# Optimization experiments

Measured on AMD Instinct MI355X. Metric: run time of the kernel, lower is better.

## Reference

```python
import jax, jax.numpy as jnp
import numpy as np

B = 512          # batch of graphs
N_LOCAL = 33     # local nodes per graph
NPG = 34         # nodes per graph (1 global + 33 local)
C = 768          # feat_dims[-1] (global feature channels)
FEAT = 1152      # concat_dim = sum(feat_dims) = 384 + 768
GPD = 2048       # global_proj_dim
HID = 1024       # hidden_dim_proj
H = 8            # num_heads
AD = 64          # att_dim
LLM = 4096       # llama_dim
DEG = 8          # average degree of random graph
E_PER = NPG * DEG
NT = B * NPG     # total nodes


def setup_inputs() -> dict:
    key = jax.random.key(0)
    ks = jax.random.split(key, 16)
    sc = 0.02
    local_features = jax.random.normal(ks[0], (B, 1, N_LOCAL, FEAT), jnp.float32)
    global_features = jax.random.normal(ks[1], (B, C, 8, 8, 4), jnp.float32)
    # random batched graph: edges stay within each graph, offset by 34*b
    src = jax.random.randint(ks[2], (B, E_PER), 0, NPG)
    dst = jax.random.randint(ks[3], (B, E_PER), 0, NPG)
    off = (jnp.arange(B, dtype=jnp.int32) * NPG)[:, None]
    edge_index = jnp.stack([(src + off).reshape(-1), (dst + off).reshape(-1)]).astype(jnp.int32)
    return {
        "local_features": local_features,
        "global_features": global_features,
        "edge_index": edge_index,
        "W1g": jax.random.normal(ks[4], (32 * C, GPD), jnp.float32) * sc,
        "b1g": jnp.zeros((GPD,), jnp.float32),
        "W2g": jax.random.normal(ks[5], (GPD, FEAT), jnp.float32) * sc,
        "b2g": jnp.zeros((FEAT,), jnp.float32),
        "Wp": jax.random.normal(ks[6], (FEAT, HID), jnp.float32) * sc,
        "bp": jnp.zeros((HID,), jnp.float32),
        "Wg": jax.random.normal(ks[7], (HID, H * AD), jnp.float32) * sc,
        "a_src": jax.random.normal(ks[8], (H, AD), jnp.float32) * sc,
        "a_dst": jax.random.normal(ks[9], (H, AD), jnp.float32) * sc,
        "Wllm": jax.random.normal(ks[10], (H * AD, LLM), jnp.float32) * sc,
        "bllm": jnp.zeros((LLM,), jnp.float32),
    }


def reference(local_features, global_features, edge_index,
              W1g, b1g, W2g, b2g, Wp, bp, Wg, a_src, a_dst, Wllm, bllm):
    # AdaptiveAvgPool3d((4,4,2)) on (8,8,4): exact 2x2x2 mean pooling
    x = global_features.reshape(B, C, 4, 2, 4, 2, 2, 2).mean(axis=(3, 5, 7))
    x = x.reshape(B, -1)                                   # [B, 32*C]
    out_global = jax.nn.relu(x @ W1g + b1g) @ W2g + b2g    # [B, FEAT]
    # concat global node with local nodes -> [B, 34, FEAT] -> flatten batched graph
    nodes = jnp.concatenate([out_global[:, None, :], local_features[:, 0]], axis=1)
    nodes = nodes.reshape(NT, FEAT)

    # GAT layer: hidden projection, per-head features, edge attention
    h = jax.nn.relu(nodes @ Wp + bp)                       # [NT, HID]
    z = (h @ Wg).reshape(NT, H, AD)                        # [NT, H, AD]
    s, d = edge_index[0], edge_index[1]
    e = jax.nn.leaky_relu(
        jnp.einsum('ehd,hd->eh', z[s], a_src) + jnp.einsum('ehd,hd->eh', z[d], a_dst),
        negative_slope=0.2)                                # [E, H]
    m = jax.ops.segment_max(e, d, num_segments=NT)
    m = jnp.where(jnp.isfinite(m), m, 0.0)                 # guard isolated nodes
    ex = jnp.exp(e - m[d])
    den = jax.ops.segment_sum(ex, d, num_segments=NT)
    alpha = ex / (den[d] + 1e-9)                           # neighbor softmax per dst
    agg = jax.ops.segment_sum(alpha[:, :, None] * z[s], d, num_segments=NT)  # [NT, H, AD]
    gnn_feats = agg.reshape(NT, H * AD)

    out = gnn_feats.reshape(B, NPG, H * AD) @ Wllm + bllm  # [B, 34, LLM]
    return out
```

## Files before the change

### kernel.cpp

```cpp
#include <hip/hip_runtime.h>
#include <hip/hip_bf16.h>
#include <math.h>

#define BB    512
#define NPG   34
#define NT    17408
#define FEAT  1152
#define GPD   2048
#define HID   1024
#define NH    8
#define AD    64
#define HA    512
#define LLM   4096
#define EPG   272
#define NE    139264
#define C32   24576
#define CC    768

#define AS3 __attribute__((address_space(3)))
#define AS1 __attribute__((address_space(1)))

typedef __attribute__((ext_vector_type(8))) short short8v;
typedef __attribute__((ext_vector_type(4))) float f32x4;

__device__ __forceinline__ ushort f2bf(float f) {
    __hip_bfloat16 h = __float2bfloat16(f);
    return __builtin_bit_cast(ushort, h);
}

__device__ __forceinline__ void d_transpose(const float* __restrict__ W, ushort* __restrict__ WT,
                                            int R, int Cn, int bx, int by,
                                            float (*tile)[33], int tid) {
    int c0 = bx * 32, r0 = by * 32;
    int tc = tid & 31, tr = tid >> 5;
#pragma unroll
    for (int i = 0; i < 4; i++)
        tile[tr + i * 8][tc] = W[(size_t)(r0 + tr + i * 8) * Cn + c0 + tc];
    __syncthreads();
#pragma unroll
    for (int it = 0; it < 2; it++) {
        int p = tid + it * 256;
        int c = p >> 4, pr = (p & 15) << 1;
        ushort2 v;
        v.x = f2bf(tile[pr][c]);
        v.y = f2bf(tile[pr + 1][c]);
        *(ushort2*)&WT[(size_t)(c0 + c) * R + r0 + pr] = v;
    }
}

__device__ __forceinline__ void d_pool(const float* __restrict__ gf, ushort* __restrict__ outB,
                                       int blk, int tid) {
    int t = blk * 256 + tid;
    int q = t & 15; int bc = t >> 4;
    int dO = q >> 2, hO = q & 3;
    const float* p = gf + (size_t)bc * 256 + dO * 64 + hO * 8;
    float4 r00 = *(const float4*)(p);
    float4 r01 = *(const float4*)(p + 4);
    float4 r10 = *(const float4*)(p + 32);
    float4 r11 = *(const float4*)(p + 36);
    float o0 = (r00.x + r00.y + r01.x + r01.y + r10.x + r10.y + r11.x + r11.y) * 0.125f;
    float o1 = (r00.z + r00.w + r01.z + r01.w + r10.z + r10.w + r11.z + r11.w) * 0.125f;
    int b = bc / CC, c = bc % CC;
    ushort2 v; v.x = f2bf(o0); v.y = f2bf(o1);
    *(ushort2*)(outB + (size_t)b * C32 + c * 32 + dO * 8 + hO * 2) = v;
}

__global__ __launch_bounds__(256) void k_prep(
    const float* __restrict__ W1g, ushort* __restrict__ W1gT,
    const float* __restrict__ W2g, ushort* __restrict__ W2gT,
    const float* __restrict__ Wp,  ushort* __restrict__ WpT,
    const float* __restrict__ Wg,  ushort* __restrict__ WgT,
    const float* __restrict__ Wllm, ushort* __restrict__ WllmT,
    const float* __restrict__ gf,  ushort* __restrict__ poolB) {
    __shared__ float tile[32][33];
    int blk = blockIdx.x, tid = threadIdx.x;
    if (blk < 49152) {
        d_transpose(W1g, W1gT, C32, GPD, blk & 63, blk >> 6, tile, tid);
    } else if (blk < 51456) {
        int l = blk - 49152; d_transpose(W2g, W2gT, GPD, FEAT, l % 36, l / 36, tile, tid);
    } else if (blk < 52608) {
        int l = blk - 51456; d_transpose(Wp, WpT, FEAT, HID, l & 31, l >> 5, tile, tid);
    } else if (blk < 53120) {
        int l = blk - 52608; d_transpose(Wg, WgT, HID, HA, l & 15, l >> 4, tile, tid);
    } else if (blk < 55168) {
        int l = blk - 53120; d_transpose(Wllm, WllmT, HA, LLM, l & 127, l >> 7, tile, tid);
    } else {
        d_pool(gf, poolB, blk - 55168, tid);
    }
}

#define GLDS(gp, lp) __builtin_amdgcn_global_load_lds((const AS1 void*)(gp), (AS3 void*)(lp), 16, 0, 0)
#define STAGE_A(buf, h, tt) { \
    const ushort* s_ = gAs + (size_t)(tt) * 64 + (size_t)(2 * (h)) * rK; \
    ushort* d_ = lds + (buf) * 32768 + (2 * (h)) * 4096 + (w << 9); \
    GLDS(s_, d_); GLDS(s_ + rK, d_ + 4096); }
#define STAGE_B(buf, h, tt) { \
    const ushort* s_ = gBs + (size_t)(tt) * 64 + (size_t)(2 * (h)) * rK; \
    ushort* d_ = lds + (buf) * 32768 + 16384 + (2 * (h)) * 4096 + (w << 9); \
    GLDS(s_, d_); GLDS(s_ + rK, d_ + 4096); }
#define DSRA(BO, mh) { _Pragma("unroll") for (int mf = 0; mf < 4; mf++) { \
    const ushort* p_ = lds + (BO) + aBase + ((mh) * 64 + mf * 16) * 64; \
    aF[mf][0] = *(const short8v*)(p_ + k0s); \
    aF[mf][1] = *(const short8v*)(p_ + k1s); } }
#define DSRB(BO, nh, BF) { _Pragma("unroll") for (int nf = 0; nf < 2; nf++) { \
    const ushort* p_ = lds + (BO) + bBase + ((nh) * 32 + nf * 16) * 64; \
    BF[nf][0] = *(const short8v*)(p_ + k0s); \
    BF[nf][1] = *(const short8v*)(p_ + k1s); } }
#define MM(mh, nh, BF) { \
    asm volatile("s_waitcnt lgkmcnt(0)" ::: "memory"); \
    __builtin_amdgcn_sched_barrier(0); \
    __builtin_amdgcn_s_setprio(1); \
    _Pragma("unroll") for (int mf = 0; mf < 4; mf++) \
    _Pragma("unroll") for (int nf = 0; nf < 2; nf++) { \
        acc[(mh)*4+mf][(nh)*2+nf] = __builtin_amdgcn_mfma_f32_16x16x32_bf16(aF[mf][0], BF[nf][0], acc[(mh)*4+mf][(nh)*2+nf], 0, 0, 0); \
        acc[(mh)*4+mf][(nh)*2+nf] = __builtin_amdgcn_mfma_f32_16x16x32_bf16(aF[mf][1], BF[nf][1], acc[(mh)*4+mf][(nh)*2+nf], 0, 0, 0); } \
    __builtin_amdgcn_s_setprio(0); }
#define BAR __builtin_amdgcn_s_barrier()
#define VMW4 { asm volatile("s_waitcnt vmcnt(4)" ::: "memory"); __builtin_amdgcn_sched_barrier(0); }

template<bool SPLITK, bool BIAS, bool RELU, bool OUTBF>
__global__ __launch_bounds__(512, 2) void k_gemm256(
    const ushort* __restrict__ A, const ushort* __restrict__ BT,
    const float* __restrict__ bias, void* __restrict__ Cout,
    int M, int N, int K, int kChunk) {
    __shared__ ushort lds[65536];
    const int t = threadIdx.x;
    const int w = t >> 6, l = t & 63;
    const int wm = w >> 2, wn = w & 3;
    const int gx = gridDim.x;
    const int nwg = gx * gridDim.y;
    const int id = blockIdx.y * gx + blockIdx.x;
    const int qx = nwg >> 3, rx = nwg & 7;
    const int xcd = id & 7, pos = id >> 3;
    const int nid = (xcd < rx ? xcd * (qx + 1) : rx * (qx + 1) + (xcd - rx) * qx) + pos;
    const int m0 = (nid / gx) * 256, n0 = (nid % gx) * 256;
    const int kBase = SPLITK ? blockIdx.z * kChunk : 0;
    const int NTt = (SPLITK ? kChunk : K) / 64;

    const int rowLo = t >> 3;
    const int keSrc = ((t & 7) << 3) ^ (((rowLo >> 2) & 1) << 5) ^ (((rowLo >> 3) & 1) << 4);
    const ushort* gAs = A + (size_t)(m0 + rowLo) * K + kBase + keSrc;
    const ushort* gBs = BT + (size_t)(n0 + rowLo) * K + kBase + keSrc;
    const size_t rK = (size_t)64 * K;

    const int fcol = l & 15, fk = (l >> 4) << 3;
    const int flipR = (((l >> 2) & 1) << 5) | (((l >> 3) & 1) << 4);
    const int k0s = fk ^ flipR;
    const int k1s = fk ^ 32 ^ flipR;
    const int aBase = (wm * 128 + fcol) * 64;
    const int bBase = 16384 + (wn * 64 + fcol) * 64;

    short8v aF[4][2], bF0[2][2], bF1[2][2];
    f32x4 acc[8][4] = {};

    STAGE_B(0, 0, 0); STAGE_B(0, 1, 0); STAGE_A(0, 0, 0); STAGE_A(0, 1, 0);
    STAGE_B(1, 0, 1); STAGE_B(1, 1, 1);
    VMW4;
    BAR;

    const int NITER = NTt >> 1;
    for (int it = 0; it < NITER; ++it) {
        const int t1 = 2 * it + 1;
        const int t2r = 2 * it + 2, t3r = 2 * it + 3;
        const int t2 = t2r < NTt ? t2r : 0;
        const int t3 = t3r < NTt ? t3r : 0;
        DSRA(0, 0); DSRB(0, 0, bF0); STAGE_A(1, 0, t1);
        BAR; MM(0, 0, bF0); BAR;
        DSRB(0, 1, bF1); STAGE_A(1, 1, t1);
        BAR; MM(0, 1, bF1); BAR;
        DSRA(0, 1); STAGE_B(0, 0, t2);
        BAR; MM(1, 1, bF1); BAR;
        STAGE_B(0, 1, t2); VMW4;
        BAR; MM(1, 0, bF0); BAR;
        DSRA(32768, 0); DSRB(32768, 0, bF0); STAGE_A(0, 0, t2);
        BAR; MM(0, 0, bF0); BAR;
        DSRB(32768, 1, bF1); STAGE_A(0, 1, t2);
        BAR; MM(0, 1, bF1); BAR;
        DSRA(32768, 1); STAGE_B(1, 0, t3);
        BAR; MM(1, 1, bF1); BAR;
        STAGE_B(1, 1, t3); VMW4;
        BAR; MM(1, 0, bF0); BAR;
    }
    asm volatile("s_waitcnt vmcnt(0)" ::: "memory");
    BAR;

    const int orow = (l >> 4) << 2;
    float* eph = ((float*)lds) + w * 2176;
    const int ecol = (l & 15) << 2;
    const int erow4 = l >> 4;
#pragma unroll
    for (int pass = 0; pass < 4; pass++) {
#pragma unroll
        for (int mi = 0; mi < 2; mi++) {
            int mf = pass * 2 + mi;
#pragma unroll
            for (int nf = 0; nf < 4; nf++)
#pragma unroll
                for (int r = 0; r < 4; r++)
                    eph[(mi * 16 + orow + r) * 68 + nf * 16 + fcol] = acc[mf][nf][r];
        }
#pragma unroll
        for (int g = 0; g < 8; g++) {
            int lrow = g * 4 + erow4;
            f32x4 v = *(f32x4*)&eph[lrow * 68 + ecol];
            int row = m0 + wm * 128 + pass * 32 + lrow;
            int col = n0 + wn * 64 + ecol;
            if (BIAS) {
                float4 bb = *(const float4*)(bias + col);
                v[0] += bb.x; v[1] += bb.y; v[2] += bb.z; v[3] += bb.w;
            }
            if (RELU) {
#pragma unroll
                for (int q = 0; q < 4; q++) v[q] = v[q] > 0.f ? v[q] : 0.f;
            }
            if (OUTBF) {
                ushort4 u;
                u.x = f2bf(v[0]); u.y = f2bf(v[1]); u.z = f2bf(v[2]); u.w = f2bf(v[3]);
                *(ushort4*)&((ushort*)Cout)[(size_t)row * N + col] = u;
            } else {
                size_t off = (size_t)row * N + col;
                if (SPLITK) off += (size_t)blockIdx.z * (size_t)M * N;
                float4 fv = {v[0], v[1], v[2], v[3]};
                *(float4*)&((float*)Cout)[off] = fv;
            }
        }
    }
}

template<bool SPLITK, bool BIAS, bool RELU, bool OUTBF>
__global__ __launch_bounds__(256) void k_gemm_bf(
    const ushort* __restrict__ A, const ushort* __restrict__ BT,
    const float* __restrict__ bias, void* __restrict__ Cout,
    int M, int N, int K, int kChunk) {
    __shared__ ushort lA[128 * 32];
    __shared__ ushort lB[128 * 32];
    const int t = threadIdx.x;
    const int w = t >> 6, l = t & 63;
    const int m0 = blockIdx.y * 128, n0 = blockIdx.x * 128;
    const int kLen = SPLITK ? kChunk : K;
    const int k0 = SPLITK ? blockIdx.z * kChunk : 0;
    const int srow = w * 16 + (l >> 2);
    const int skq = (l & 3) << 3;
    const ushort* gA = A + (size_t)(m0 + srow) * K + k0 + skq;
    const ushort* gB = BT + (size_t)(n0 + srow) * K + k0 + skq;
    ushort* lA0 = lA + w * 512;
    ushort* lB0 = lB + w * 512;
    const size_t str64 = (size_t)64 * K;
    const int wr = (w >> 1) << 6, wc = (w & 1) << 6;
    const int fcol = l & 15, fk = (l >> 4) << 3;

    f32x4 acc[4][4] = {};
    for (int kk = 0; kk < kLen; kk += 32) {
        __syncthreads();
        GLDS(gA + kk,         lA0);
        GLDS(gA + kk + str64, lA0 + 2048);
        GLDS(gB + kk,         lB0);
        GLDS(gB + kk + str64, lB0 + 2048);
        __syncthreads();
        short8v a[4], b[4];
#pragma unroll
        for (int f = 0; f < 4; f++) {
            a[f] = *(const short8v*)(lA + (wr + f * 16 + fcol) * 32 + fk);
            b[f] = *(const short8v*)(lB + (wc + f * 16 + fcol) * 32 + fk);
        }
#pragma unroll
        for (int i = 0; i < 4; i++)
#pragma unroll
            for (int j = 0; j < 4; j++)
                acc[i][j] = __builtin_amdgcn_mfma_f32_16x16x32_bf16(a[i], b[j], acc[i][j], 0, 0, 0);
    }
    const int orow = (l >> 4) << 2;
#pragma unroll
    for (int i = 0; i < 4; i++) {
#pragma unroll
        for (int j = 0; j < 4; j++) {
            int col = n0 + wc + j * 16 + fcol;
            float bv = BIAS ? bias[col] : 0.f;
#pragma unroll
            for (int r = 0; r < 4; r++) {
                int row = m0 + wr + i * 16 + orow + r;
                float v = acc[i][j][r] + bv;
                if (RELU) v = v > 0.f ? v : 0.f;
                if (OUTBF) {
                    ((ushort*)Cout)[(size_t)row * N + col] = f2bf(v);
                } else {
                    size_t off = (size_t)row * N + col;
                    if (SPLITK) off += (size_t)blockIdx.z * (size_t)M * N;
                    ((float*)Cout)[off] = v;
                }
            }
        }
    }
}

template<int NP, bool RELU>
__global__ __launch_bounds__(256) void k_red(const float* __restrict__ part,
                                             const float* __restrict__ bias,
                                             ushort* __restrict__ outB,
                                             int N, int stride) {
    int i = blockIdx.x * 256 + threadIdx.x;
    float s = bias[i % N];
#pragma unroll
    for (int q = 0; q < NP; q++) s += part[i + (size_t)q * stride];
    if (RELU) s = s > 0.f ? s : 0.f;
    outB[i] = f2bf(s);
}

__global__ __launch_bounds__(256) void k_nodes(const ushort* __restrict__ outgB,
                                               const float* __restrict__ locf,
                                               ushort* __restrict__ nodesB) {
    int idx = blockIdx.x * 256 + threadIdx.x;
    int node = idx / 144, cc = idx - node * 144;
    int b = node / NPG, j = node - b * NPG;
    int c = cc * 8;
    ushort* dst = nodesB + (size_t)node * FEAT + c;
    if (j == 0) {
        *(uint4*)dst = *(const uint4*)(outgB + (size_t)b * FEAT + c);
    } else {
        const float* s = locf + ((size_t)b * 33 + (j - 1)) * FEAT + c;
        float4 v0 = *(const float4*)s, v1 = *(const float4*)(s + 4);
        ushort u[8] = {f2bf(v0.x), f2bf(v0.y), f2bf(v0.z), f2bf(v0.w),
                       f2bf(v1.x), f2bf(v1.y), f2bf(v1.z), f2bf(v1.w)};
        *(uint4*)dst = *(uint4*)u;
    }
}

__global__ __launch_bounds__(256) void k_gat(const int* __restrict__ es, const int* __restrict__ ed,
                                             const float* __restrict__ z,
                                             const float* __restrict__ a_src,
                                             const float* __restrict__ a_dst,
                                             ushort* __restrict__ gnnB) {
    __shared__ float zt[NPG][520];
    __shared__ float sps[NPG][NH], spd[NPG][NH], sm[NPG][NH], sden[NPG][NH];
    __shared__ float esc[EPG][NH];
    __shared__ int srcl[EPG], dll[EPG], order[EPG], cnt[NPG], bstart[NPG + 1];
    int b = blockIdx.x, t = threadIdx.x;
    for (int i = t; i < NPG * 128; i += 256) {
        int n = i >> 7, c4 = (i & 127) << 2;
        *(float4*)&zt[n][c4] = *(const float4*)&z[((size_t)b * NPG + n) * HA + c4];
    }
    for (int e = t; e < EPG; e += 256) {
        srcl[e] = es[b * EPG + e] - b * NPG;
        dll[e]  = ed[b * EPG + e] - b * NPG;
    }
    if (t < NPG) cnt[t] = 0;
    __syncthreads();
    {
        int wv = t >> 6, l = t & 63;
        for (int n = wv; n < NPG; n += 4) {
            float s[NH], d[NH];
#pragma unroll
            for (int i = 0; i < NH; i++) {
                float zv = zt[n][i * 64 + l];
                s[i] = zv * a_src[i * 64 + l];
                d[i] = zv * a_dst[i * 64 + l];
            }
#pragma unroll
            for (int i = 0; i < NH; i++) {
#pragma unroll
                for (int off = 32; off > 0; off >>= 1) {
                    s[i] += __shfl_xor(s[i], off);
                    d[i] += __shfl_xor(d[i], off);
                }
            }
            if (l == 0) {
#pragma unroll
                for (int i = 0; i < NH; i++) { sps[n][i] = s[i]; spd[n][i] = d[i]; }
            }
        }
    }
    for (int e = t; e < EPG; e += 256) atomicAdd(&cnt[dll[e]], 1);
    __syncthreads();
    if (t == 0) {
        int s = 0;
        for (int n = 0; n < NPG; n++) { bstart[n] = s; s += cnt[n]; cnt[n] = bstart[n]; }
        bstart[NPG] = s;
        for (int e = 0; e < EPG; e++) order[cnt[dll[e]]++] = e;
    }
    __syncthreads();
    for (int i = t; i < EPG * NH; i += 256) {
        int e = i >> 3, h = i & 7;
        float sc = sps[srcl[e]][h] + spd[dll[e]][h];
        esc[e][h] = sc > 0.f ? sc : 0.2f * sc;
    }
    __syncthreads();
    for (int i = t; i < NPG * NH; i += 256) {
        int n = i >> 3, h = i & 7;
        float m = -INFINITY;
        for (int j = bstart[n]; j < bstart[n + 1]; j++) m = fmaxf(m, esc[order[j]][h]);
        if (m == -INFINITY) m = 0.f;
        float den = 0.f;
        for (int j = bstart[n]; j < bstart[n + 1]; j++) den += expf(esc[order[j]][h] - m);
        sm[n][h] = m; sden[n][h] = den;
    }
    __syncthreads();
    for (int i = t; i < EPG * NH; i += 256) {
        int e = i >> 3, h = i & 7;
        esc[e][h] = expf(esc[e][h] - sm[dll[e]][h]) / (sden[dll[e]][h] + 1e-9f);
    }
    __syncthreads();
    for (int c = t; c < NPG * 64; c += 256) {
        int n = c >> 6, rem = c & 63, h = rem >> 3, d0 = (rem & 7) << 3;
        float acc[8] = {};
        for (int j = bstart[n]; j < bstart[n + 1]; j++) {
            int e = order[j];
            float a = esc[e][h];
            const float* zp = &zt[srcl[e]][h * 64 + d0];
#pragma unroll
            for (int q = 0; q < 8; q++) acc[q] = fmaf(a, zp[q], acc[q]);
        }
        ushort u[8];
#pragma unroll
        for (int q = 0; q < 8; q++) u[q] = f2bf(acc[q]);
        *(uint4*)&gnnB[((size_t)b * NPG + n) * HA + h * 64 + d0] = *(uint4*)u;
    }
}

extern "C" void kernel_launch(void* const* d_in, const int* in_sizes, int n_in,
                              void* d_out, int out_size, void* d_ws, size_t ws_size,
                              hipStream_t stream) {
    const float* locf  = (const float*)d_in[0];
    const float* gf    = (const float*)d_in[1];
    const int*   ei    = (const int*)d_in[2];
    const float* W1g   = (const float*)d_in[3];
    const float* b1g   = (const float*)d_in[4];
    const float* W2g   = (const float*)d_in[5];
    const float* b2g   = (const float*)d_in[6];
    const float* Wp    = (const float*)d_in[7];
    const float* bp    = (const float*)d_in[8];
    const float* Wg    = (const float*)d_in[9];
    const float* a_src = (const float*)d_in[10];
    const float* a_dst = (const float*)d_in[11];
    const float* Wllm  = (const float*)d_in[12];
    const float* bllm  = (const float*)d_in[13];
    float* out = (float*)d_out;
    float* ws  = (float*)d_ws;
    const int* es = ei;
    const int* ed = ei + NE;

    float*  z      = out;
    ushort* W1gT   = (ushort*)(out + 8912896);
    ushort* hB     = (ushort*)(out + 8912896);
    ushort* poolB  = (ushort*)(out + 34078720);
    float*  part1  = out + 40370176;
    ushort* nodesB = (ushort*)(out + 40370176);
    ushort* g1B    = (ushort*)(out + 57147392);
    ushort* W2gT   = (ushort*)(out + 57671680);
    ushort* WpT    = (ushort*)(out + 58851328);
    ushort* WgT    = (ushort*)(out + 59441152);
    ushort* outgB  = (ushort*)(out + 59703296);
    float*  part2  = out + 59998208;
    ushort* WllmT = (ushort*)ws;
    ushort* gnnB  = (ushort*)(ws + 1048576);

    k_prep<<<79744, 256, 0, stream>>>(W1g, W1gT, W2g, W2gT, Wp, WpT, Wg, WgT,
                                      Wllm, WllmT, gf, poolB);
    k_gemm256<true, false, false, false><<<dim3(8, 2, 16), 512, 0, stream>>>(
        poolB, W1gT, nullptr, part1, 512, GPD, C32, 1536);
    k_red<16, true><<<4096, 256, 0, stream>>>(part1, b1g, g1B, GPD, 1048576);
    k_gemm_bf<true, false, false, false><<<dim3(9, 4, 4), 256, 0, stream>>>(
        g1B, W2gT, nullptr, part2, 512, FEAT, GPD, 512);
    k_red<4, false><<<2304, 256, 0, stream>>>(part2, b2g, outgB, FEAT, 589824);
    k_nodes<<<9792, 256, 0, stream>>>(outgB, locf, nodesB);
    k_gemm256<false, true, true, true><<<dim3(4, 68), 512, 0, stream>>>(
        nodesB, WpT, bp, hB, NT, HID, FEAT, 0);
    k_gemm256<false, false, false, false><<<dim3(2, 68), 512, 0, stream>>>(
        hB, WgT, nullptr, z, NT, HA, HID, 0);
    k_gat<<<BB, 256, 0, stream>>>(es, ed, z, a_src, a_dst, gnnB);
    k_gemm256<false, true, false, false><<<dim3(16, 68), 512, 0, stream>>>(
        gnnB, WllmT, bllm, out, NT, LLM, HA, 0);
}
```

Measured before the change: 595.2 us.

## Fuse z projection GEMM into GAT kernel and remap split-K block order

Replaces the separate h@Wg GEMM and the fp32 z round trip through global memory with an in-block MFMA projection. Each graph's 34 rows are multiplied by WgT directly into LDS inside a new 512-thread GAT kernel. The split-K GEMM also gets a z-major XCD-aware block remapping so that K-chunk blocks sharing output tiles are grouped. The fused projection pads 34 rows to 48 and streams WgT from global per block without LDS staging, so it wastes some MFMA work and re-reads WgT 512 times.

```diff
diff --git a/kernel.cpp b/kernel.cpp
--- a/kernel.cpp
+++ b/kernel.cpp
@@ -118,7 +118,7 @@
 #define BAR __builtin_amdgcn_s_barrier()
 #define VMW4 { asm volatile("s_waitcnt vmcnt(4)" ::: "memory"); __builtin_amdgcn_sched_barrier(0); }
 
-template<bool SPLITK, bool BIAS, bool RELU, bool OUTBF>
+template<bool SPLITK, bool ZMAJ, bool BIAS, bool RELU, bool OUTBF>
 __global__ __launch_bounds__(512, 2) void k_gemm256(
     const ushort* __restrict__ A, const ushort* __restrict__ BT,
     const float* __restrict__ bias, void* __restrict__ Cout,
@@ -127,14 +127,29 @@
     const int t = threadIdx.x;
     const int w = t >> 6, l = t & 63;
     const int wm = w >> 2, wn = w & 3;
-    const int gx = gridDim.x;
-    const int nwg = gx * gridDim.y;
-    const int id = blockIdx.y * gx + blockIdx.x;
-    const int qx = nwg >> 3, rx = nwg & 7;
-    const int xcd = id & 7, pos = id >> 3;
-    const int nid = (xcd < rx ? xcd * (qx + 1) : rx * (qx + 1) + (xcd - rx) * qx) + pos;
-    const int m0 = (nid / gx) * 256, n0 = (nid % gx) * 256;
-    const int kBase = SPLITK ? blockIdx.z * kChunk : 0;
+    int m0, n0, kz = 0;
+    {
+        const int gx = gridDim.x, gy = gridDim.y;
+        if (ZMAJ) {
+            const int nwg = gx * gy * gridDim.z;
+            const int id = (blockIdx.z * gx + blockIdx.x) * gy + blockIdx.y;
+            const int qc = nwg >> 3, rc = nwg & 7;
+            const int xcd = id & 7, pos = id >> 3;
+            const int nid = (xcd < rc ? xcd * (qc + 1) : rc * (qc + 1) + (xcd - rc) * qc) + pos;
+            const int y = nid % gy; const int r2 = nid / gy;
+            const int x = r2 % gx; kz = r2 / gx;
+            m0 = y * 256; n0 = x * 256;
+        } else {
+            const int nwg = gx * gy;
+            const int id = blockIdx.y * gx + blockIdx.x;
+            const int qc = nwg >> 3, rc = nwg & 7;
+            const int xcd = id & 7, pos = id >> 3;
+            const int nid = (xcd < rc ? xcd * (qc + 1) : rc * (qc + 1) + (xcd - rc) * qc) + pos;
+            m0 = (nid / gx) * 256; n0 = (nid % gx) * 256;
+            kz = blockIdx.z;
+        }
+    }
+    const int kBase = SPLITK ? kz * kChunk : 0;
     const int NTt = (SPLITK ? kChunk : K) / 64;
 
     const int rowLo = t >> 3;
@@ -219,7 +234,7 @@
                 *(ushort4*)&((ushort*)Cout)[(size_t)row * N + col] = u;
             } else {
                 size_t off = (size_t)row * N + col;
-                if (SPLITK) off += (size_t)blockIdx.z * (size_t)M * N;
+                if (SPLITK) off += (size_t)kz * (size_t)M * N;
                 float4 fv = {v[0], v[1], v[2], v[3]};
                 *(float4*)&((float*)Cout)[off] = fv;
             }
@@ -325,51 +340,89 @@
     }
 }
 
-__global__ __launch_bounds__(256) void k_gat(const int* __restrict__ es, const int* __restrict__ ed,
-                                             const float* __restrict__ z,
-                                             const float* __restrict__ a_src,
-                                             const float* __restrict__ a_dst,
-                                             ushort* __restrict__ gnnB) {
-    __shared__ float zt[NPG][520];
-    __shared__ float sps[NPG][NH], spd[NPG][NH], sm[NPG][NH], sden[NPG][NH];
+__global__ __launch_bounds__(512) void k_zgat(const int* __restrict__ es, const int* __restrict__ ed,
+                                              const ushort* __restrict__ hB,
+                                              const ushort* __restrict__ WgT,
+                                              const float* __restrict__ a_src,
+                                              const float* __restrict__ a_dst,
+                                              ushort* __restrict__ gnnB) {
+    __shared__ float zt[NPG][521];
+    __shared__ float sps[NPG][NH], spd[NPG][NH], smx[NPG][NH], sden[NPG][NH];
     __shared__ float esc[EPG][NH];
     __shared__ int srcl[EPG], dll[EPG], order[EPG], cnt[NPG], bstart[NPG + 1];
-    int b = blockIdx.x, t = threadIdx.x;
-    for (int i = t; i < NPG * 128; i += 256) {
-        int n = i >> 7, c4 = (i & 127) << 2;
-        *(float4*)&zt[n][c4] = *(const float4*)&z[((size_t)b * NPG + n) * HA + c4];
-    }
-    for (int e = t; e < EPG; e += 256) {
+    const int b = blockIdx.x, t = threadIdx.x;
+    const int w = t >> 6, l = t & 63;
+    const int lm = l & 15, lh = l >> 4;
+
+    f32x4 acc[3][4] = {};
+    const ushort* hrow[3];
+    bool hval[3];
+#pragma unroll
+    for (int mi = 0; mi < 3; mi++) {
+        int row = mi * 16 + lm;
+        hval[mi] = row < NPG;
+        hrow[mi] = hB + ((size_t)b * NPG + (hval[mi] ? row : 0)) * HID + lh * 8;
+    }
+    const ushort* brow[4];
+#pragma unroll
+    for (int q = 0; q < 4; q++)
+        brow[q] = WgT + (size_t)((w * 4 + q) * 16 + lm) * HID + lh * 8;
+    const short8v zerov = {};
+#pragma unroll 2
+    for (int ks = 0; ks < 32; ks++) {
+        const int kb = ks * 32;
+        short8v af[3], bf[4];
+#pragma unroll
+        for (int mi = 0; mi < 3; mi++) {
+            short8v v = *(const short8v*)(hrow[mi] + kb);
+            af[mi] = hval[mi] ? v : zerov;
+        }
+#pragma unroll
+        for (int q = 0; q < 4; q++) bf[q] = *(const short8v*)(brow[q] + kb);
+#pragma unroll
+        for (int mi = 0; mi < 3; mi++)
+#pragma unroll
+            for (int q = 0; q < 4; q++)
+                acc[mi][q] = __builtin_amdgcn_mfma_f32_16x16x32_bf16(af[mi], bf[q], acc[mi][q], 0, 0, 0);
+    }
+#pragma unroll
+    for (int mi = 0; mi < 3; mi++)
+#pragma unroll
+        for (int q = 0; q < 4; q++)
+#pragma unroll
+            for (int r = 0; r < 4; r++) {
+                int m = mi * 16 + lh * 4 + r;
+                if (m < NPG) zt[m][(w * 4 + q) * 16 + lm] = acc[mi][q][r];
+            }
+    for (int e = t; e < EPG; e += 512) {
         srcl[e] = es[b * EPG + e] - b * NPG;
         dll[e]  = ed[b * EPG + e] - b * NPG;
     }
     if (t < NPG) cnt[t] = 0;
     __syncthreads();
-    {
-        int wv = t >> 6, l = t & 63;
-        for (int n = wv; n < NPG; n += 4) {
-            float s[NH], d[NH];
-#pragma unroll
-            for (int i = 0; i < NH; i++) {
-                float zv = zt[n][i * 64 + l];
-                s[i] = zv * a_src[i * 64 + l];
-                d[i] = zv * a_dst[i * 64 + l];
+
+    for (int n = w; n < NPG; n += 8) {
+        float s[NH], d[NH];
+#pragma unroll
+        for (int i = 0; i < NH; i++) {
+            float zv = zt[n][i * 64 + l];
+            s[i] = zv * a_src[i * 64 + l];
+            d[i] = zv * a_dst[i * 64 + l];
+        }
+#pragma unroll
+        for (int i = 0; i < NH; i++) {
+#pragma unroll
+            for (int off = 32; off > 0; off >>= 1) {
+                s[i] += __shfl_xor(s[i], off);
+                d[i] += __shfl_xor(d[i], off);
             }
-#pragma unroll
-            for (int i = 0; i < NH; i++) {
-#pragma unroll
-                for (int off = 32; off > 0; off >>= 1) {
-                    s[i] += __shfl_xor(s[i], off);
-                    d[i] += __shfl_xor(d[i], off);
-                }
-            }
-            if (l == 0) {
-#pragma unroll
-                for (int i = 0; i < NH; i++) { sps[n][i] = s[i]; spd[n][i] = d[i]; }
-            }
-        }
-    }
-    for (int e = t; e < EPG; e += 256) atomicAdd(&cnt[dll[e]], 1);
+        }
+        if (l == 0) {
+#pragma unroll
+            for (int i = 0; i < NH; i++) { sps[n][i] = s[i]; spd[n][i] = d[i]; }
+        }
+    }
+    for (int e = t; e < EPG; e += 512) atomicAdd(&cnt[dll[e]], 1);
     __syncthreads();
     if (t == 0) {
         int s = 0;
@@ -378,40 +431,40 @@
         for (int e = 0; e < EPG; e++) order[cnt[dll[e]]++] = e;
     }
     __syncthreads();
-    for (int i = t; i < EPG * NH; i += 256) {
+    for (int i = t; i < EPG * NH; i += 512) {
         int e = i >> 3, h = i & 7;
         float sc = sps[srcl[e]][h] + spd[dll[e]][h];
         esc[e][h] = sc > 0.f ? sc : 0.2f * sc;
     }
     __syncthreads();
-    for (int i = t; i < NPG * NH; i += 256) {
+    for (int i = t; i < NPG * NH; i += 512) {
         int n = i >> 3, h = i & 7;
         float m = -INFINITY;
         for (int j = bstart[n]; j < bstart[n + 1]; j++) m = fmaxf(m, esc[order[j]][h]);
         if (m == -INFINITY) m = 0.f;
         float den = 0.f;
         for (int j = bstart[n]; j < bstart[n + 1]; j++) den += expf(esc[order[j]][h] - m);
-        sm[n][h] = m; sden[n][h] = den;
-    }
-    __syncthreads();
-    for (int i = t; i < EPG * NH; i += 256) {
+        smx[n][h] = m; sden[n][h] = den;
+    }
+    __syncthreads();
+    for (int i = t; i < EPG * NH; i += 512) {
         int e = i >> 3, h = i & 7;
-        esc[e][h] = expf(esc[e][h] - sm[dll[e]][h]) / (sden[dll[e]][h] + 1e-9f);
-    }
-    __syncthreads();
-    for (int c = t; c < NPG * 64; c += 256) {
+        esc[e][h] = expf(esc[e][h] - smx[dll[e]][h]) / (sden[dll[e]][h] + 1e-9f);
+    }
+    __syncthreads();
+    for (int c = t; c < NPG * 64; c += 512) {
         int n = c >> 6, rem = c & 63, h = rem >> 3, d0 = (rem & 7) << 3;
-        float acc[8] = {};
+        float a8[8] = {};
         for (int j = bstart[n]; j < bstart[n + 1]; j++) {
             int e = order[j];
             float a = esc[e][h];
             const float* zp = &zt[srcl[e]][h * 64 + d0];
 #pragma unroll
-            for (int q = 0; q < 8; q++) acc[q] = fmaf(a, zp[q], acc[q]);
+            for (int q = 0; q < 8; q++) a8[q] = fmaf(a, zp[q], a8[q]);
         }
         ushort u[8];
 #pragma unroll
-        for (int q = 0; q < 8; q++) u[q] = f2bf(acc[q]);
+        for (int q = 0; q < 8; q++) u[q] = f2bf(a8[q]);
         *(uint4*)&gnnB[((size_t)b * NPG + n) * HA + h * 64 + d0] = *(uint4*)u;
     }
 }
@@ -438,7 +491,6 @@
     const int* es = ei;
     const int* ed = ei + NE;
 
-    float*  z      = out;
     ushort* W1gT   = (ushort*)(out + 8912896);
     ushort* hB     = (ushort*)(out + 8912896);
     ushort* poolB  = (ushort*)(out + 34078720);
@@ -455,18 +507,16 @@
 
     k_prep<<<79744, 256, 0, stream>>>(W1g, W1gT, W2g, W2gT, Wp, WpT, Wg, WgT,
                                       Wllm, WllmT, gf, poolB);
-    k_gemm256<true, false, false, false><<<dim3(8, 2, 16), 512, 0, stream>>>(
+    k_gemm256<true, true, false, false, false><<<dim3(8, 2, 16), 512, 0, stream>>>(
         poolB, W1gT, nullptr, part1, 512, GPD, C32, 1536);
     k_red<16, true><<<4096, 256, 0, stream>>>(part1, b1g, g1B, GPD, 1048576);
     k_gemm_bf<true, false, false, false><<<dim3(9, 4, 4), 256, 0, stream>>>(
         g1B, W2gT, nullptr, part2, 512, FEAT, GPD, 512);
     k_red<4, false><<<2304, 256, 0, stream>>>(part2, b2g, outgB, FEAT, 589824);
     k_nodes<<<9792, 256, 0, stream>>>(outgB, locf, nodesB);
-    k_gemm256<false, true, true, true><<<dim3(4, 68), 512, 0, stream>>>(
+    k_gemm256<false, false, true, true, true><<<dim3(4, 68), 512, 0, stream>>>(
         nodesB, WpT, bp, hB, NT, HID, FEAT, 0);
-    k_gemm256<false, false, false, false><<<dim3(2, 68), 512, 0, stream>>>(
-        hB, WgT, nullptr, z, NT, HA, HID, 0);
-    k_gat<<<BB, 256, 0, stream>>>(es, ed, z, a_src, a_dst, gnnB);
-    k_gemm256<false, true, false, false><<<dim3(16, 68), 512, 0, stream>>>(
+    k_zgat<<<BB, 512, 0, stream>>>(es, ed, hB, WgT, a_src, a_dst, gnnB);
+    k_gemm256<false, false, true, false, false><<<dim3(16, 68), 512, 0, stream>>>(
         gnnB, WllmT, bllm, out, NT, LLM, HA, 0);
 }
```

New measurement: 645.8 us. +8.5%, slower.
